# Kernel optimization log

Measured on AMD Instinct MI355X. Metric: run time of the kernel, lower is better.

Reference implementation:

```python
import jax, jax.numpy as jnp
import numpy as np

DIM = 1024
MLP_DIM = 4096
EPS = 1e-5


def layer_norm(x, gamma, beta):
    mean = jnp.mean(x, axis=-1, keepdims=True)
    var = jnp.mean(jnp.square(x - mean), axis=-1, keepdims=True)  # unbiased=False
    return gamma * (x - mean) / jnp.sqrt(var + EPS) + beta


def setup_inputs() -> dict:
    key = jax.random.key(0)
    ks = jax.random.split(key, 12)
    s = 0.02
    return {
        "x": jax.random.normal(ks[0], (4, 2048, DIM), dtype=jnp.float32),
        "gamma1": jnp.ones((DIM,), jnp.float32),
        "beta1": jnp.zeros((DIM,), jnp.float32),
        "gamma2": jnp.ones((DIM,), jnp.float32),
        "beta2": jnp.zeros((DIM,), jnp.float32),
        "Wq": jax.random.normal(ks[1], (DIM, DIM), jnp.float32) * s,
        "bq": jnp.zeros((DIM,), jnp.float32),
        "Wk": jax.random.normal(ks[2], (DIM, DIM), jnp.float32) * s,
        "bk": jnp.zeros((DIM,), jnp.float32),
        "Wv": jax.random.normal(ks[3], (DIM, DIM), jnp.float32) * s,
        "bv": jnp.zeros((DIM,), jnp.float32),
        "W1": jax.random.normal(ks[4], (DIM, MLP_DIM), jnp.float32) * s,
        "b1": jnp.zeros((MLP_DIM,), jnp.float32),
        "W2": jax.random.normal(ks[5], (MLP_DIM, DIM), jnp.float32) * s,
        "b2": jnp.zeros((DIM,), jnp.float32),
    }


def reference(x, gamma1, beta1, gamma2, beta2, Wq, bq, Wk, bk, Wv, bv, W1, b1, W2, b2):
    # Pre-LN attention sub-block (single-head manual attention over full dim)
    residual = x
    h = layer_norm(x, gamma1, beta1)
    q = h @ Wq + bq  # [B,S,D]
    k = h @ Wk + bk
    v = h @ Wv + bv
    scale = 1.0 / jnp.sqrt(jnp.asarray(q.shape[-1], q.dtype))
    scores = jnp.einsum("bsd,btd->bst", q, k) * scale  # [B,S,S]
    attn = jax.nn.softmax(scores, axis=-1)
    x = jnp.einsum("bst,btd->bsd", attn, v) + residual
    # Pre-LN MLP sub-block
    residual = x
    h = layer_norm(x, gamma2, beta2)
    h = jax.nn.gelu(h @ W1 + b1, approximate=False)  # torch F.gelu exact
    x = h @ W2 + b2 + residual
    return x
```

## Files before the change

kernel.cpp:

```cpp
#include <hip/hip_runtime.h>
#include <hip/hip_bf16.h>
#include <math.h>

typedef __bf16 bf16x8 __attribute__((ext_vector_type(8)));
typedef float  f32x4  __attribute__((ext_vector_type(4)));
typedef __hip_bfloat16 bf16;

#define DIM  1024
#define MLPD 4096
#define NB   4
#define SEQ  2048
#define ROWS (NB * SEQ)

__device__ __forceinline__ void gload_lds16(const void* g, void* l) {
  __builtin_amdgcn_global_load_lds(
      (__attribute__((address_space(1))) void*)(g),
      (__attribute__((address_space(3))) void*)(l), 16, 0, 0);
}

__device__ __forceinline__ void bar() {
  asm volatile("" ::: "memory");
  __builtin_amdgcn_s_barrier();
  asm volatile("" ::: "memory");
}

template <int N>
__device__ __forceinline__ void vmw() {
  asm volatile("s_waitcnt vmcnt(%0)" ::"n"(N) : "memory");
}

__device__ __forceinline__ bf16 to_bf16(float v) { return __float2bfloat16(v); }
__device__ __forceinline__ bf16 to_bf16(bf16 v)  { return v; }

__device__ __forceinline__ float gelu_exact_fast(float v) {
  const float x  = v * 0.70710678118654752f;
  const float ax = fabsf(x);
  const float t  = __builtin_amdgcn_rcpf(1.0f + 0.3275911f * ax);
  const float p  = t * (0.254829592f +
                   t * (-0.284496736f +
                   t * (1.421413741f +
                   t * (-1.453152027f + t * 1.061405429f))));
  float erf = 1.0f - p * __expf(-x * x);
  erf = copysignf(erf, x);
  return 0.5f * v * (1.0f + erf);
}

template <int EPI>
__global__ __launch_bounds__(512, 2) void gemm256(
    const bf16* __restrict__ A,  long aBatch, int lda,
    const bf16* __restrict__ Bt, long bBatch, int ldb,
    void* __restrict__ Cout,     long cBatch, int ldc,
    const float* __restrict__ bias, int K, float scale)
{
  extern __shared__ char smem[];

  const int gx = gridDim.x, gy = gridDim.y;
  int flat = blockIdx.x + gx * (blockIdx.y + gy * blockIdx.z);
  const int nwg = gx * gy * gridDim.z;
  flat = (flat & 7) * (nwg >> 3) + (flat >> 3);
  const int bx = flat % gx;
  const int t2 = flat / gx;
  const int by = t2 % gy;
  const int bz = t2 / gy;

  const long rowBase = (long)by * 256;
  const long colBase = (long)bx * 256;
  const long ldaB = (long)lda * 2, ldbB = (long)ldb * 2;
  const char* Ag = (const char*)(A + bz * aBatch + rowBase * lda);
  const char* Bg = (const char*)(Bt + bz * bBatch + colBase * ldb);

  const int tid  = threadIdx.x;
  const int lane = tid & 63;
  const int wave = tid >> 6;
  const int wm = wave >> 2, wn = wave & 3;
  const int fr = lane & 15, fq = lane >> 4;
  const int fh2 = fr >> 1;
  const int sA = (((fr & 1) << 2) | fq) ^ fh2;
  const int rdCom = fh2 * 128 + sA * 16;

  long offA[2], offB[2];
#pragma unroll
  for (int li = 0; li < 2; ++li) {
    const int d = li * 512 + tid;
    {
      const int wms = d >> 9, kks = (d >> 8) & 1, w = d & 255;
      const int pr = w >> 3, s = w & 7, u = s ^ (pr & 7);
      offA[li] = (long)(wms * 128 + pr * 2 + (u >> 2)) * ldaB +
                 kks * 64 + (u & 3) * 16;
    }
    {
      const int wns = d >> 8, kkb = (d >> 7) & 1, w = d & 127;
      const int pr = w >> 3, s = w & 7, u = s ^ (pr & 7);
      offB[li] = (long)(wns * 64 + pr * 2 + (u >> 2)) * ldbB +
                 kkb * 64 + (u & 3) * 16;
    }
  }
  const int dstOff = tid * 16;
  const long aHalf = ldaB << 6;
  const long bHalf = ldbB << 5;

  const int NT = K >> 6;

  bf16x8 a[4][2], b[2][2][2];
  f32x4 acc[8][4] = {};

#define STG_A(J, mh)                                                           \
  do {                                                                         \
    char* _d = smem + (((J) & 1) << 16) + (mh) * 16384 + dstOff;               \
    const char* _s = Ag + (J) * 128 + (mh) * aHalf;                            \
    gload_lds16(_s + offA[0], _d);                                             \
    gload_lds16(_s + offA[1], _d + 8192);                                      \
  } while (0)

#define STG_B(J, nh)                                                           \
  do {                                                                         \
    char* _d = smem + (((J) & 1) << 16) + 32768 + (nh) * 16384 + dstOff;       \
    const char* _s = Bg + (J) * 128 + (nh) * bHalf;                            \
    gload_lds16(_s + offB[0], _d);                                             \
    gload_lds16(_s + offB[1], _d + 8192);                                      \
  } while (0)

#define LDA(mh, J)                                                             \
  do {                                                                         \
    const char* _b = smem + (((J) & 1) << 16) + (mh) * 16384 + wm * 8192 +     \
                     rdCom;                                                    \
    _Pragma("unroll") for (int m = 0; m < 4; ++m)                              \
      _Pragma("unroll") for (int kk = 0; kk < 2; ++kk)                         \
        a[m][kk] = *(const bf16x8*)(_b + kk * 4096 + m * 1024);                \
  } while (0)

#define LDB(nh, J)                                                             \
  do {                                                                         \
    const char* _b = smem + (((J) & 1) << 16) + 32768 + (nh) * 16384 +         \
                     wn * 4096 + rdCom;                                        \
    _Pragma("unroll") for (int n = 0; n < 2; ++n)                              \
      _Pragma("unroll") for (int kk = 0; kk < 2; ++kk)                         \
        b[nh][n][kk] = *(const bf16x8*)(_b + kk * 2048 + n * 1024);            \
  } while (0)

#define MM(mh, nh)                                                             \
  do {                                                                         \
    __builtin_amdgcn_s_setprio(1);                                             \
    _Pragma("unroll") for (int m = 0; m < 4; ++m)                              \
      _Pragma("unroll") for (int n = 0; n < 2; ++n)                            \
        _Pragma("unroll") for (int kk = 0; kk < 2; ++kk)                       \
          acc[(mh) * 4 + m][(nh) * 2 + n] =                                    \
              __builtin_amdgcn_mfma_f32_16x16x32_bf16(                         \
                  a[m][kk], b[nh][n][kk], acc[(mh) * 4 + m][(nh) * 2 + n],     \
                  0, 0, 0);                                                    \
    __builtin_amdgcn_s_setprio(0);                                             \
  } while (0)

#define LGKM0 asm volatile("s_waitcnt lgkmcnt(0)" ::: "memory")

#define TILE(J, S1, S2, VN)                                                    \
  do {                                                                         \
    LDA(0, J); LDB(0, J);                                                      \
    if (S1) STG_A((J) + 1, 1);                                                 \
    bar(); LGKM0; MM(0, 0); bar();                                             \
    LDB(1, J);                                                                 \
    if (S2) STG_A((J) + 2, 0);                                                 \
    bar(); LGKM0; MM(0, 1); bar();                                             \
    LDA(1, J);                                                                 \
    if (S2) STG_B((J) + 2, 0);                                                 \
    bar(); LGKM0; MM(1, 1); bar();                                             \
    if (S2) STG_B((J) + 2, 1);                                                 \
    vmw<VN>(); bar(); MM(1, 0); bar();                                         \
  } while (0)

  STG_A(0, 0); STG_B(0, 0); STG_B(0, 1); STG_A(0, 1);
  STG_A(1, 0); STG_B(1, 0); STG_B(1, 1);
  vmw<6>(); bar();

  for (int j = 0; j < NT - 2; ++j) TILE(j, true, true, 6);
  TILE(NT - 2, true, false, 0);
  TILE(NT - 1, false, false, 63);

#undef STG_A
#undef STG_B
#undef LDA
#undef LDB
#undef MM
#undef TILE

#pragma unroll
  for (int mh = 0; mh < 2; ++mh)
#pragma unroll
    for (int m = 0; m < 4; ++m)
#pragma unroll
      for (int nh = 0; nh < 2; ++nh)
#pragma unroll
        for (int n = 0; n < 2; ++n) {
          const long col = colBase + wn * 64 + nh * 32 + n * 16 + fr;
#pragma unroll
          for (int e = 0; e < 4; ++e) {
            const long r = rowBase + wm * 128 + mh * 64 + m * 16 + fq * 4 + e;
            float v = acc[mh * 4 + m][nh * 2 + n][e];
            if constexpr (EPI == 0) {
              v += bias[col];
              ((bf16*)Cout)[bz * cBatch + r * ldc + col] = __float2bfloat16(v);
            } else {
              ((bf16*)Cout)[bz * cBatch + r * ldc + col] =
                  __float2bfloat16(v * scale);
            }
          }
        }
}

template <int EPI>
__global__ __launch_bounds__(256, 4) void gemm128(
    const bf16* __restrict__ A,  long aBatch, int lda,
    const bf16* __restrict__ Bt, long bBatch, int ldb,
    void* __restrict__ Cout,     long cBatch, int ldc,
    const float* __restrict__ bias,
    const float* __restrict__ resid, long rBatch, int ldr,
    int K, float scale)
{
  __shared__ char smem[2][16384];

  const int gx = gridDim.x, gy = gridDim.y;
  const int n = gx * gy * gridDim.z;
  const int f = blockIdx.x + gx * (blockIdx.y + gy * blockIdx.z);
  const int o = (f & 7) * (n >> 3) + (f >> 3);
  const int sx = gx >> 3;
  int st = o >> 6;
  const int w = o & 63;
  const int spz = sx * (gy >> 3);
  const int bz = st / spz; st -= bz * spz;
  const int sty = st / sx, stx = st - sty * sx;
  const int by = sty * 8 + (w >> 3), bx = stx * 8 + (w & 7);

  const long rowBase = (long)by * 128;
  const long colBase = (long)bx * 128;
  const long ldaB = (long)lda * 2, ldbB = (long)ldb * 2;
  const char* Ag = (const char*)(A + bz * aBatch + rowBase * lda);
  const char* Bg = (const char*)(Bt + bz * bBatch + colBase * ldb);

  const int tid  = threadIdx.x;
  const int lane = tid & 63;
  const int wave = tid >> 6;
  const int wm = wave >> 1, wn = wave & 1;
  const int fr = lane & 15, fq = lane >> 4;

  const int fh = fr >> 1;
  const int sA = (((fr & 1) << 2) | fq) ^ fh;
  const int laneRd = fh * 128 + sA * 16;
  const int abase = wm * 4096 + laneRd;
  const int bbase = 8192 + wn * 4096 + laneRd;

  const int t0   = wave * 128 + lane;
  const int r2   = t0 >> 3;
  const int u0   = (t0 & 7) ^ (r2 & 7);
  const int row0 = r2 * 2 + (u0 >> 2);
  const int kc0  = u0 & 3;
  const char* aSrc0 = Ag + (long)row0 * ldaB + kc0 * 16;
  const char* aSrc1 = aSrc0 + 16 * ldaB;
  const char* bSrc0 = Bg + (long)row0 * ldbB + kc0 * 16;
  const char* bSrc1 = bSrc0 + 16 * ldbB;
  const int doff = wave * 2048 + lane * 16;

  const int NT = K >> 5;
  f32x4 acc[4][4] = {};

#define STAGE(WB)                                                              \
  do {                                                                         \
    gload_lds16(aSrc0, &smem[WB][doff]);                                       \
    gload_lds16(aSrc1, &smem[WB][doff + 1024]);                                \
    gload_lds16(bSrc0, &smem[WB][8192 + doff]);                                \
    gload_lds16(bSrc1, &smem[WB][8192 + doff + 1024]);                         \
    aSrc0 += 64; aSrc1 += 64; bSrc0 += 64; bSrc1 += 64;                        \
  } while (0)

#define READMM(RB)                                                             \
  do {                                                                         \
    const char* _r = &smem[RB][0];                                             \
    bf16x8 av[4], bv[4];                                                       \
    _Pragma("unroll") for (int m = 0; m < 4; ++m)                              \
      av[m] = *(const bf16x8*)(_r + abase + m * 1024);                         \
    _Pragma("unroll") for (int nn = 0; nn < 4; ++nn)                           \
      bv[nn] = *(const bf16x8*)(_r + bbase + nn * 1024);                       \
    __builtin_amdgcn_s_setprio(1);                                             \
    _Pragma("unroll") for (int m = 0; m < 4; ++m)                              \
      _Pragma("unroll") for (int nn = 0; nn < 4; ++nn)                         \
        acc[m][nn] = __builtin_amdgcn_mfma_f32_16x16x32_bf16(                  \
            av[m], bv[nn], acc[m][nn], 0, 0, 0);                               \
    __builtin_amdgcn_s_setprio(0);                                             \
  } while (0)

  for (int t = 0; t < NT; t += 2) {
    STAGE(0);
    STAGE(1);
    vmw<0>(); bar();
    READMM(0);
    READMM(1);
    bar();
  }

#undef STAGE
#undef READMM

#pragma unroll
  for (int m = 0; m < 4; ++m) {
#pragma unroll
    for (int nn = 0; nn < 4; ++nn) {
      const long col = colBase + wn * 64 + nn * 16 + fr;
#pragma unroll
      for (int e = 0; e < 4; ++e) {
        const long r = rowBase + wm * 64 + m * 16 + fq * 4 + e;
        float v = acc[m][nn][e];
        if constexpr (EPI == 2) {
          v += resid[bz * rBatch + r * ldr + col];
          ((float*)Cout)[bz * cBatch + r * ldc + col] = v;
        } else if constexpr (EPI == 3) {
          v += bias[col];
          ((bf16*)Cout)[bz * cBatch + r * ldc + col] =
              __float2bfloat16(gelu_exact_fast(v));
        } else {
          v += bias[col] + resid[r * (long)ldr + col];
          ((float*)Cout)[bz * cBatch + r * ldc + col] = v;
        }
      }
    }
  }
}

__global__ __launch_bounds__(256) void ln_kernel(
    const float* __restrict__ x, const float* __restrict__ gamma,
    const float* __restrict__ beta, bf16* __restrict__ out)
{
  const long row = blockIdx.x;
  const float4 v = ((const float4*)(x + row * DIM))[threadIdx.x];
  float s  = v.x + v.y + v.z + v.w;
  float ss = v.x * v.x + v.y * v.y + v.z * v.z + v.w * v.w;
  const int lane = threadIdx.x & 63, wave = threadIdx.x >> 6;
#pragma unroll
  for (int o = 32; o; o >>= 1) { s += __shfl_xor(s, o); ss += __shfl_xor(ss, o); }
  __shared__ float rs[4], rss[4];
  if (lane == 0) { rs[wave] = s; rss[wave] = ss; }
  __syncthreads();
  s  = rs[0] + rs[1] + rs[2] + rs[3];
  ss = rss[0] + rss[1] + rss[2] + rss[3];
  const float mean = s * (1.0f / DIM);
  const float var  = ss * (1.0f / DIM) - mean * mean;
  const float rstd = rsqrtf(var + 1e-5f);
  const float4 g = ((const float4*)gamma)[threadIdx.x];
  const float4 b = ((const float4*)beta)[threadIdx.x];
  union { bf16 h[4]; uint2 u; } pk;
  pk.h[0] = __float2bfloat16(g.x * (v.x - mean) * rstd + b.x);
  pk.h[1] = __float2bfloat16(g.y * (v.y - mean) * rstd + b.y);
  pk.h[2] = __float2bfloat16(g.z * (v.z - mean) * rstd + b.z);
  pk.h[3] = __float2bfloat16(g.w * (v.w - mean) * rstd + b.w);
  ((uint2*)(out + row * DIM))[threadIdx.x] = pk.u;
}

__global__ __launch_bounds__(256) void softmax_kernel(bf16* __restrict__ scores)
{
  const long row = blockIdx.x;
  bf16* rp = scores + row * (long)SEQ;
  union { bf16 h[8]; uint4 u; } in;
  in.u = ((const uint4*)rp)[threadIdx.x];
  float f[8];
#pragma unroll
  for (int j = 0; j < 8; ++j) f[j] = __bfloat162float(in.h[j]);
  const int lane = threadIdx.x & 63, wave = threadIdx.x >> 6;
  float mx = f[0];
#pragma unroll
  for (int j = 1; j < 8; ++j) mx = fmaxf(mx, f[j]);
#pragma unroll
  for (int o = 32; o; o >>= 1) mx = fmaxf(mx, __shfl_xor(mx, o));
  __shared__ float rm[4], rsum[4];
  if (lane == 0) rm[wave] = mx;
  __syncthreads();
  mx = fmaxf(fmaxf(rm[0], rm[1]), fmaxf(rm[2], rm[3]));
  float sum = 0.0f;
#pragma unroll
  for (int j = 0; j < 8; ++j) { f[j] = expf(f[j] - mx); sum += f[j]; }
#pragma unroll
  for (int o = 32; o; o >>= 1) sum += __shfl_xor(sum, o);
  if (lane == 0) rsum[wave] = sum;
  __syncthreads();
  sum = rsum[0] + rsum[1] + rsum[2] + rsum[3];
  const float inv = 1.0f / sum;
  union { bf16 h[8]; uint4 u; } pk;
#pragma unroll
  for (int j = 0; j < 8; ++j) pk.h[j] = __float2bfloat16(f[j] * inv);
  ((uint4*)rp)[threadIdx.x] = pk.u;
}

__global__ __launch_bounds__(256) void transpose_v_kernel(
    const bf16* __restrict__ in, bf16* __restrict__ out,
    int ldIn, int ldOut, long inBatch, long outBatch)
{
  __shared__ bf16 tile[32][33];
  const long zin  = (long)blockIdx.z * inBatch;
  const long zout = (long)blockIdx.z * outBatch;
  const int c0 = blockIdx.x * 32, r0 = blockIdx.y * 32;
  const int tx = threadIdx.x & 31, ty = threadIdx.x >> 5;
#pragma unroll
  for (int i = 0; i < 32; i += 8)
    tile[ty + i][tx] = in[zin + (long)(r0 + ty + i) * ldIn + c0 + tx];
  __syncthreads();
#pragma unroll
  for (int i = 0; i < 32; i += 8)
    out[zout + (long)(c0 + ty + i) * ldOut + r0 + tx] = tile[tx][ty + i];
}

__global__ __launch_bounds__(256) void prep_kernel(
    const float* __restrict__ Wq, const float* __restrict__ Wk,
    const float* __restrict__ Wv, const float* __restrict__ W1,
    const float* __restrict__ W2,
    const float* __restrict__ bq, const float* __restrict__ bk,
    const float* __restrict__ bv,
    bf16* __restrict__ WqkvT, bf16* __restrict__ W1T,
    bf16* __restrict__ W2T, float* __restrict__ bqkv)
{
  int l = blockIdx.x;
  if (l >= 11264) {
    const int i = (l - 11264) * 256 + threadIdx.x;
    bqkv[i] = bq[i]; bqkv[DIM + i] = bk[i]; bqkv[2 * DIM + i] = bv[i];
    return;
  }
  __shared__ bf16 tile[32][33];
  const float* in; bf16* out; int ldIn, ldOut, gxw;
  if (l < 3072) {
    const int wsel = l / 1024;
    in = (wsel == 0) ? Wq : (wsel == 1) ? Wk : Wv;
    out = WqkvT + (long)wsel * DIM * DIM;
    l &= 1023; ldIn = DIM; ldOut = DIM; gxw = 32;
  } else if (l < 7168) {
    in = W1; out = W1T; l -= 3072; ldIn = MLPD; ldOut = DIM; gxw = 128;
  } else {
    in = W2; out = W2T; l -= 7168; ldIn = DIM; ldOut = MLPD; gxw = 32;
  }
  const int bxx = l % gxw, byy = l / gxw;
  const int c0 = bxx * 32, r0 = byy * 32;
  const int tx = threadIdx.x & 31, ty = threadIdx.x >> 5;
#pragma unroll
  for (int i = 0; i < 32; i += 8)
    tile[ty + i][tx] = __float2bfloat16(in[(long)(r0 + ty + i) * ldIn + c0 + tx]);
  __syncthreads();
#pragma unroll
  for (int i = 0; i < 32; i += 8)
    out[(long)(c0 + ty + i) * ldOut + r0 + tx] = tile[tx][ty + i];
}

extern "C" void kernel_launch(void* const* d_in, const int* in_sizes, int n_in,
                              void* d_out, int out_size, void* d_ws, size_t ws_size,
                              hipStream_t stream) {
  const float* x   = (const float*)d_in[0];
  const float* g1  = (const float*)d_in[1];
  const float* be1 = (const float*)d_in[2];
  const float* g2  = (const float*)d_in[3];
  const float* be2 = (const float*)d_in[4];
  const float* Wq  = (const float*)d_in[5];
  const float* bq  = (const float*)d_in[6];
  const float* Wk  = (const float*)d_in[7];
  const float* bk  = (const float*)d_in[8];
  const float* Wv  = (const float*)d_in[9];
  const float* bv  = (const float*)d_in[10];
  const float* W1  = (const float*)d_in[11];
  const float* b1  = (const float*)d_in[12];
  const float* W2  = (const float*)d_in[13];
  const float* b2  = (const float*)d_in[14];
  float* out = (float*)d_out;

  char* ws = (char*)d_ws;
  bf16* WqkvT = (bf16*)(ws + 0);
  bf16* W1T   = (bf16*)(ws + (6l << 20));
  bf16* W2T   = (bf16*)(ws + (14l << 20));
  float* bqkv = (float*)(ws + (22l << 20));
  bf16* h     = (bf16*)(ws + (23l << 20));
  bf16* qkv   = (bf16*)(ws + (39l << 20));
  bf16* vT    = (bf16*)(ws + (87l << 20));
  bf16* sc    = (bf16*)(ws + (103l << 20));
  bf16* g_act = (bf16*)sc;

  const int SMEM = 131072;
  hipFuncSetAttribute(reinterpret_cast<const void*>(&gemm256<0>),
                      hipFuncAttributeMaxDynamicSharedMemorySize, SMEM);
  hipFuncSetAttribute(reinterpret_cast<const void*>(&gemm256<5>),
                      hipFuncAttributeMaxDynamicSharedMemorySize, SMEM);

  const dim3 blk(256), gblk(512);

  prep_kernel<<<11268, blk, 0, stream>>>(Wq, Wk, Wv, W1, W2, bq, bk, bv,
                                         WqkvT, W1T, W2T, bqkv);

  ln_kernel<<<ROWS, blk, 0, stream>>>(x, g1, be1, h);

  gemm256<0><<<dim3(12, 32, 1), gblk, SMEM, stream>>>(
      h, 0, DIM, WqkvT, 0, DIM, qkv, 0, 3 * DIM, bqkv, DIM, 1.0f);

  transpose_v_kernel<<<dim3(32, 64, NB), blk, 0, stream>>>(
      qkv + 2 * DIM, vT, 3 * DIM, SEQ, (long)SEQ * 3 * DIM, (long)DIM * SEQ);

  gemm256<5><<<dim3(8, 8, NB), gblk, SMEM, stream>>>(
      qkv, (long)SEQ * 3 * DIM, 3 * DIM, qkv + DIM, (long)SEQ * 3 * DIM,
      3 * DIM, sc, (long)SEQ * SEQ, SEQ, nullptr, DIM, 0.03125f);

  softmax_kernel<<<ROWS, blk, 0, stream>>>(sc);

  gemm128<2><<<dim3(8, 16, NB), blk, 0, stream>>>(
      sc, (long)SEQ * SEQ, SEQ, vT, (long)DIM * SEQ, SEQ,
      out, (long)SEQ * DIM, DIM, nullptr, x, (long)SEQ * DIM, DIM, SEQ, 1.0f);

  ln_kernel<<<ROWS, blk, 0, stream>>>(out, g2, be2, h);

  gemm128<3><<<dim3(32, 64, 1), blk, 0, stream>>>(
      h, 0, DIM, W1T, 0, DIM, g_act, 0, MLPD, b1, nullptr, 0, 0, DIM, 1.0f);

  gemm128<4><<<dim3(8, 64, 1), blk, 0, stream>>>(
      g_act, 0, MLPD, W2T, 0, MLPD, out, 0, DIM, b2, out, 0, DIM, MLPD, 1.0f);
}
```

Before: 363.0 us.

## Compute V transposed directly via swapped GEMM and fuse LN1 into prep kernel

Computes V^T directly as Wv^T·h^T with a new gemm128 epilogue that adds a per-row bias and writes bf16. This removes the separate transpose kernel and its extra read and write of the V tensor. The QK projection now covers only 2*DIM columns, and the first layernorm is folded into the weight-prep launch as extra blocks, saving one kernel launch. The swapped GEMM writes its output with a strided pattern and uses a different tile shape, which may be less efficient than the fused QKV GEMM.

```diff
diff --git a/kernel.cpp b/kernel.cpp
--- a/kernel.cpp
+++ b/kernel.cpp
@@ -28,9 +28,6 @@
 __device__ __forceinline__ void vmw() {
   asm volatile("s_waitcnt vmcnt(%0)" ::"n"(N) : "memory");
 }
-
-__device__ __forceinline__ bf16 to_bf16(float v) { return __float2bfloat16(v); }
-__device__ __forceinline__ bf16 to_bf16(bf16 v)  { return v; }
 
 __device__ __forceinline__ float gelu_exact_fast(float v) {
   const float x  = v * 0.70710678118654752f;
@@ -274,16 +271,16 @@
 #define READMM(RB)                                                             \
   do {                                                                         \
     const char* _r = &smem[RB][0];                                             \
-    bf16x8 av[4], bv[4];                                                       \
+    bf16x8 av[4], bv_[4];                                                      \
     _Pragma("unroll") for (int m = 0; m < 4; ++m)                              \
       av[m] = *(const bf16x8*)(_r + abase + m * 1024);                         \
     _Pragma("unroll") for (int nn = 0; nn < 4; ++nn)                           \
-      bv[nn] = *(const bf16x8*)(_r + bbase + nn * 1024);                       \
+      bv_[nn] = *(const bf16x8*)(_r + bbase + nn * 1024);                      \
     __builtin_amdgcn_s_setprio(1);                                             \
     _Pragma("unroll") for (int m = 0; m < 4; ++m)                              \
       _Pragma("unroll") for (int nn = 0; nn < 4; ++nn)                         \
         acc[m][nn] = __builtin_amdgcn_mfma_f32_16x16x32_bf16(                  \
-            av[m], bv[nn], acc[m][nn], 0, 0, 0);                               \
+            av[m], bv_[nn], acc[m][nn], 0, 0, 0);                              \
     __builtin_amdgcn_s_setprio(0);                                             \
   } while (0)
 
@@ -315,9 +312,12 @@
           v += bias[col];
           ((bf16*)Cout)[bz * cBatch + r * ldc + col] =
               __float2bfloat16(gelu_exact_fast(v));
-        } else {
+        } else if constexpr (EPI == 4) {
           v += bias[col] + resid[r * (long)ldr + col];
           ((float*)Cout)[bz * cBatch + r * ldc + col] = v;
+        } else {
+          v += bias[r];
+          ((bf16*)Cout)[bz * cBatch + r * ldc + col] = __float2bfloat16(v);
         }
       }
     }
@@ -387,46 +387,58 @@
   ((uint4*)rp)[threadIdx.x] = pk.u;
 }
 
-__global__ __launch_bounds__(256) void transpose_v_kernel(
-    const bf16* __restrict__ in, bf16* __restrict__ out,
-    int ldIn, int ldOut, long inBatch, long outBatch)
-{
-  __shared__ bf16 tile[32][33];
-  const long zin  = (long)blockIdx.z * inBatch;
-  const long zout = (long)blockIdx.z * outBatch;
-  const int c0 = blockIdx.x * 32, r0 = blockIdx.y * 32;
-  const int tx = threadIdx.x & 31, ty = threadIdx.x >> 5;
-#pragma unroll
-  for (int i = 0; i < 32; i += 8)
-    tile[ty + i][tx] = in[zin + (long)(r0 + ty + i) * ldIn + c0 + tx];
-  __syncthreads();
-#pragma unroll
-  for (int i = 0; i < 32; i += 8)
-    out[zout + (long)(c0 + ty + i) * ldOut + r0 + tx] = tile[tx][ty + i];
-}
-
 __global__ __launch_bounds__(256) void prep_kernel(
     const float* __restrict__ Wq, const float* __restrict__ Wk,
     const float* __restrict__ Wv, const float* __restrict__ W1,
     const float* __restrict__ W2,
     const float* __restrict__ bq, const float* __restrict__ bk,
-    const float* __restrict__ bv,
-    bf16* __restrict__ WqkvT, bf16* __restrict__ W1T,
-    bf16* __restrict__ W2T, float* __restrict__ bqkv)
+    const float* __restrict__ x, const float* __restrict__ g1,
+    const float* __restrict__ be1,
+    bf16* __restrict__ WqkT, bf16* __restrict__ WvT,
+    bf16* __restrict__ W1T, bf16* __restrict__ W2T,
+    float* __restrict__ bqk, bf16* __restrict__ hOut)
 {
   int l = blockIdx.x;
+  if (l >= 11268) {
+    const long row = l - 11268;
+    const float4 v = ((const float4*)(x + row * DIM))[threadIdx.x];
+    float s  = v.x + v.y + v.z + v.w;
+    float ss = v.x * v.x + v.y * v.y + v.z * v.z + v.w * v.w;
+    const int lane = threadIdx.x & 63, wave = threadIdx.x >> 6;
+#pragma unroll
+    for (int o = 32; o; o >>= 1) { s += __shfl_xor(s, o); ss += __shfl_xor(ss, o); }
+    __shared__ float rs[4], rss[4];
+    if (lane == 0) { rs[wave] = s; rss[wave] = ss; }
+    __syncthreads();
+    s  = rs[0] + rs[1] + rs[2] + rs[3];
+    ss = rss[0] + rss[1] + rss[2] + rss[3];
+    const float mean = s * (1.0f / DIM);
+    const float var  = ss * (1.0f / DIM) - mean * mean;
+    const float rstd = rsqrtf(var + 1e-5f);
+    const float4 g = ((const float4*)g1)[threadIdx.x];
+    const float4 b = ((const float4*)be1)[threadIdx.x];
+    union { bf16 h[4]; uint2 u; } pk;
+    pk.h[0] = __float2bfloat16(g.x * (v.x - mean) * rstd + b.x);
+    pk.h[1] = __float2bfloat16(g.y * (v.y - mean) * rstd + b.y);
+    pk.h[2] = __float2bfloat16(g.z * (v.z - mean) * rstd + b.z);
+    pk.h[3] = __float2bfloat16(g.w * (v.w - mean) * rstd + b.w);
+    ((uint2*)(hOut + row * DIM))[threadIdx.x] = pk.u;
+    return;
+  }
   if (l >= 11264) {
     const int i = (l - 11264) * 256 + threadIdx.x;
-    bqkv[i] = bq[i]; bqkv[DIM + i] = bk[i]; bqkv[2 * DIM + i] = bv[i];
+    bqk[i] = bq[i]; bqk[DIM + i] = bk[i];
     return;
   }
   __shared__ bf16 tile[32][33];
   const float* in; bf16* out; int ldIn, ldOut, gxw;
-  if (l < 3072) {
-    const int wsel = l / 1024;
-    in = (wsel == 0) ? Wq : (wsel == 1) ? Wk : Wv;
-    out = WqkvT + (long)wsel * DIM * DIM;
+  if (l < 2048) {
+    const int wsel = l >> 10;
+    in = wsel ? Wk : Wq;
+    out = WqkT + (long)wsel * DIM * DIM;
     l &= 1023; ldIn = DIM; ldOut = DIM; gxw = 32;
+  } else if (l < 3072) {
+    in = Wv; out = WvT; l -= 2048; ldIn = DIM; ldOut = DIM; gxw = 32;
   } else if (l < 7168) {
     in = W1; out = W1T; l -= 3072; ldIn = MLPD; ldOut = DIM; gxw = 128;
   } else {
@@ -465,14 +477,15 @@
   float* out = (float*)d_out;
 
   char* ws = (char*)d_ws;
-  bf16* WqkvT = (bf16*)(ws + 0);
+  bf16* WqkT  = (bf16*)(ws + 0);
+  bf16* WvT   = (bf16*)(ws + (4l << 20));
   bf16* W1T   = (bf16*)(ws + (6l << 20));
   bf16* W2T   = (bf16*)(ws + (14l << 20));
-  float* bqkv = (float*)(ws + (22l << 20));
+  float* bqk  = (float*)(ws + (22l << 20));
   bf16* h     = (bf16*)(ws + (23l << 20));
-  bf16* qkv   = (bf16*)(ws + (39l << 20));
-  bf16* vT    = (bf16*)(ws + (87l << 20));
-  bf16* sc    = (bf16*)(ws + (103l << 20));
+  bf16* qk    = (bf16*)(ws + (39l << 20));
+  bf16* vT    = (bf16*)(ws + (71l << 20));
+  bf16* sc    = (bf16*)(ws + (87l << 20));
   bf16* g_act = (bf16*)sc;
 
   const int SMEM = 131072;
@@ -483,20 +496,20 @@
 
   const dim3 blk(256), gblk(512);
 
-  prep_kernel<<<11268, blk, 0, stream>>>(Wq, Wk, Wv, W1, W2, bq, bk, bv,
-                                         WqkvT, W1T, W2T, bqkv);
-
-  ln_kernel<<<ROWS, blk, 0, stream>>>(x, g1, be1, h);
-
-  gemm256<0><<<dim3(12, 32, 1), gblk, SMEM, stream>>>(
-      h, 0, DIM, WqkvT, 0, DIM, qkv, 0, 3 * DIM, bqkv, DIM, 1.0f);
-
-  transpose_v_kernel<<<dim3(32, 64, NB), blk, 0, stream>>>(
-      qkv + 2 * DIM, vT, 3 * DIM, SEQ, (long)SEQ * 3 * DIM, (long)DIM * SEQ);
+  prep_kernel<<<11268 + ROWS, blk, 0, stream>>>(
+      Wq, Wk, Wv, W1, W2, bq, bk, x, g1, be1,
+      WqkT, WvT, W1T, W2T, bqk, h);
+
+  gemm256<0><<<dim3(8, 32, 1), gblk, SMEM, stream>>>(
+      h, 0, DIM, WqkT, 0, DIM, qk, 0, 2 * DIM, bqk, DIM, 1.0f);
+
+  gemm128<6><<<dim3(16, 8, NB), blk, 0, stream>>>(
+      WvT, 0, DIM, h, (long)SEQ * DIM, DIM,
+      vT, (long)DIM * SEQ, SEQ, bv, nullptr, 0, 0, DIM, 1.0f);
 
   gemm256<5><<<dim3(8, 8, NB), gblk, SMEM, stream>>>(
-      qkv, (long)SEQ * 3 * DIM, 3 * DIM, qkv + DIM, (long)SEQ * 3 * DIM,
-      3 * DIM, sc, (long)SEQ * SEQ, SEQ, nullptr, DIM, 0.03125f);
+      qk, (long)SEQ * 2 * DIM, 2 * DIM, qk + DIM, (long)SEQ * 2 * DIM,
+      2 * DIM, sc, (long)SEQ * SEQ, SEQ, nullptr, DIM, 0.03125f);
 
   softmax_kernel<<<ROWS, blk, 0, stream>>>(sc);
 
```

Result: faster. 348.3 us (-4.1%).
